# Optimization experiments

Hardware: AMD Instinct MI355X
Metric: run time of the kernel (lower is better)

Reference implementation:

```python
import jax, jax.numpy as jnp
import numpy as np

T, B, F, H = 1024, 128, 243, 20  # timesteps, batch, feature dim, hidden dim
POOL = 4  # MaxPool1d(4, 4) over the 512 channel axis -> 128


def setup_inputs() -> dict:
    key = jax.random.key(0)
    ks = jax.random.split(key, 9)
    s = lambda fan_in: 1.0 / np.sqrt(fan_in)
    return {
        "feats": jax.random.normal(ks[0], (T, B * POOL, F), dtype=jnp.float32),
        "e0": jax.random.normal(ks[1], (B, H), dtype=jnp.float32),
        # PyTorch GRUCell params: gates stacked as [r; z; n]
        "W_ih": jax.random.uniform(ks[2], (3 * H, F), jnp.float32, -s(H), s(H)),
        "W_hh": jax.random.uniform(ks[3], (3 * H, H), jnp.float32, -s(H), s(H)),
        "b_ih": jax.random.uniform(ks[4], (3 * H,), jnp.float32, -s(H), s(H)),
        "b_hh": jax.random.uniform(ks[5], (3 * H,), jnp.float32, -s(H), s(H)),
        # decoder: Linear(20, 243) + ReLU
        "W_dec": jax.random.uniform(ks[6], (F, H), jnp.float32, -s(H), s(H)),
        "b_dec": jax.random.uniform(ks[7], (F,), jnp.float32, -s(H), s(H)),
    }


def reference(feats, e0, W_ih, W_hh, b_ih, b_hh, W_dec, b_dec):
    # temporal max-pool over the 512 axis (kernel=4, stride=4) -> [T, B, F]
    h_seq = feats.reshape(T, B, POOL, F).max(axis=2)
    # precompute input-gate projections once (vectorized over T): [T, B, 3H]
    x_gates = jnp.einsum('tbf,gf->tbg', h_seq, W_ih) + b_ih

    def step(e, inp):
        h_t, xg = inp
        hg = e @ W_hh.T + b_hh
        xr, xz, xn = jnp.split(xg, 3, axis=-1)
        hr, hz, hn = jnp.split(hg, 3, axis=-1)
        r = jax.nn.sigmoid(xr + hr)
        z = jax.nn.sigmoid(xz + hz)
        n = jnp.tanh(xn + r * hn)
        e_new = (1.0 - z) * n + z * e
        fo = jax.nn.relu(e_new @ W_dec.T + b_dec)
        loss = jnp.mean((fo - h_t) ** 2)
        return e_new, loss

    _, losses = jax.lax.scan(step, e0, (h_seq, x_gates))
    return jnp.mean(losses)  # sum(loss_list) / step
```

## Files before the change

kernel.cpp:

```cpp
#include <hip/hip_runtime.h>
#include <cstddef>

#define T_ 1024
#define B_ 128
#define F_ 243
#define H_ 20
#define G_ 60
#define R_ 512
#define P_ 8
#define FP_ 256
#define HS_ 244

__device__ __forceinline__ float rdlane(float v, int l) {
  return __int_as_float(__builtin_amdgcn_readlane(__float_as_int(v), l));
}
#define RCP(x) __builtin_amdgcn_rcpf(x)
#if __has_builtin(__builtin_amdgcn_exp2f)
#define EXP2(x) __builtin_amdgcn_exp2f(x)
#else
#define EXP2(x) __expf((x) * 0.6931471805599453f)
#endif
#define NL2E_ -1.4426950408889634f
#define L2E2_ 2.8853900817779268f

__global__ __launch_bounds__(256) void k1a_pool(
    const float* __restrict__ feats, float* __restrict__ h_seq,
    const float* __restrict__ W_ih, float* __restrict__ Wt)
{
  const int bid = blockIdx.x;
  if (bid < 60) {
    const int i = bid * 256 + threadIdx.x;
    if (i < FP_ * G_) {
      const int f = i / G_, g = i - f * G_;
      Wt[(size_t)f * G_ + g] = (f < F_) ? W_ih[(size_t)g * F_ + f] : 0.f;
    }
  }
  const int t = bid & (T_ - 1);
  const int b0 = (bid >> 10) << 3;
  const int col = threadIdx.x;
  if (col < F_) {
    #pragma unroll
    for (int bb = 0; bb < 8; ++bb) {
      const float* p =
          feats + ((size_t)t * R_ + (size_t)(b0 + bb) * 4) * F_ + col;
      const float v =
          fmaxf(fmaxf(p[0], p[F_]), fmaxf(p[2 * F_], p[3 * F_]));
      h_seq[((size_t)(b0 + bb) * T_ + t) * HS_ + col] = v;
    }
  }
}

__global__ __launch_bounds__(256) void k1b_gemm(
    const float* __restrict__ h_seq, const float* __restrict__ Wt,
    const float* __restrict__ b_ih, float* __restrict__ xg)
{
  __shared__ __align__(16) float Ws[64 * 60];
  const int bid = blockIdx.x;
  const int b = bid >> 4;
  const int t0 = (bid & 15) << 6;
  const int tid = threadIdx.x;
  const int rg = tid >> 4;
  const int gcol = tid & 15;
  const int gc4 = (gcol < 15) ? gcol * 4 : 56;
  const float* hsb = h_seq + ((size_t)b * T_ + t0) * HS_;

  float acc[4][4];
  #pragma unroll
  for (int i = 0; i < 4; ++i)
    #pragma unroll
    for (int j = 0; j < 4; ++j) acc[i][j] = 0.f;

  for (int c = 0; c < 4; ++c) {
    const int FC = c * 64;
    __syncthreads();
    for (int j = tid; j < 64 * 60; j += 256)
      Ws[j] = Wt[(size_t)FC * G_ + j];
    __syncthreads();
    #pragma unroll
    for (int fj = 0; fj < 16; ++fj) {
      const float* wp = &Ws[(fj * 4) * 60 + gc4];
      const float4 w0 = *(const float4*)(wp);
      const float4 w1 = *(const float4*)(wp + 60);
      const float4 w2 = *(const float4*)(wp + 120);
      const float4 w3 = *(const float4*)(wp + 180);
      #pragma unroll
      for (int i = 0; i < 4; ++i) {
        const int row = (rg << 2) + i;
        const float4 a4 =
            *(const float4*)&hsb[(size_t)row * HS_ + FC + fj * 4];
        acc[i][0] = fmaf(a4.x, w0.x, fmaf(a4.y, w1.x, fmaf(a4.z, w2.x, fmaf(a4.w, w3.x, acc[i][0]))));
        acc[i][1] = fmaf(a4.x, w0.y, fmaf(a4.y, w1.y, fmaf(a4.z, w2.y, fmaf(a4.w, w3.y, acc[i][1]))));
        acc[i][2] = fmaf(a4.x, w0.z, fmaf(a4.y, w1.z, fmaf(a4.z, w2.z, fmaf(a4.w, w3.z, acc[i][2]))));
        acc[i][3] = fmaf(a4.x, w0.w, fmaf(a4.y, w1.w, fmaf(a4.z, w2.w, fmaf(a4.w, w3.w, acc[i][3]))));
      }
    }
  }

  if (gcol < 15) {
    const float4 bi4 = *(const float4*)&b_ih[gc4];
    #pragma unroll
    for (int i = 0; i < 4; ++i) {
      const int row = (rg << 2) + i;
      float4 o;
      o.x = acc[i][0] + bi4.x;  o.y = acc[i][1] + bi4.y;
      o.z = acc[i][2] + bi4.z;  o.w = acc[i][3] + bi4.w;
      *(float4*)&xg[((size_t)b * T_ + t0 + row) * G_ + gc4] = o;
    }
  }
}

__global__ __launch_bounds__(64) void k2_recur(
    const float* __restrict__ e0, const float* __restrict__ W_hh,
    const float* __restrict__ b_hh, const float* xg,
    float* e_store, float* __restrict__ ehead)
{
  const int b = blockIdx.x;
  const int lane = threadIdx.x;
  const bool own = lane < H_;
  const int j0 = own ? lane : 0;

  float2 wr2[10], wz2[10], wn2[10];
  #pragma unroll
  for (int k = 0; k < 10; ++k) {
    wr2[k] = *(const float2*)&W_hh[j0 * H_ + 2 * k];
    wz2[k] = *(const float2*)&W_hh[(j0 + 20) * H_ + 2 * k];
    wn2[k] = *(const float2*)&W_hh[(j0 + 40) * H_ + 2 * k];
  }
  const float bhr = b_hh[j0], bhz = b_hh[j0 + 20], bhn = b_hh[j0 + 40];

  float e_own = e0[b * H_ + j0];
  float2 es2[10];
  #pragma unroll
  for (int k = 0; k < 10; ++k) {
    es2[k].x = rdlane(e_own, 2 * k);
    es2[k].y = rdlane(e_own, 2 * k + 1);
  }

  const float* xgb = xg + (size_t)b * T_ * G_;
  float* xslab = e_store + (size_t)b * T_ * G_;
  float* ehb = ehead + b * (P_ * H_);

  float xr[P_], xz[P_], xn[P_];
  #pragma unroll
  for (int j = 0; j < P_; ++j) {
    xr[j] = xgb[(size_t)j * G_ + j0];
    xz[j] = xgb[(size_t)j * G_ + j0 + 20];
    xn[j] = xgb[(size_t)j * G_ + j0 + 40];
  }

#define STEP(j, RELOAD)                                                    \
  {                                                                        \
    const int t = t0 + (j);                                                \
    const float xrv = xr[j], xzv = xz[j], xnv = xn[j];                     \
    if (RELOAD) {                                                          \
      const float* xp = xgb + (size_t)(t + P_) * G_;                       \
      xr[j] = xp[j0]; xz[j] = xp[j0 + 20]; xn[j] = xp[j0 + 40];            \
    }                                                                      \
    float2 rA = make_float2(bhr, 0.f), rB = make_float2(0.f, 0.f);         \
    float2 zA = make_float2(bhz, 0.f), zB = make_float2(0.f, 0.f);         \
    float2 nA = make_float2(bhn, 0.f), nB = make_float2(0.f, 0.f);         \
    _Pragma("unroll")                                                      \
    for (int k = 0; k < 5; ++k) {                                          \
      rA = wr2[k] * es2[k] + rA;   rB = wr2[k + 5] * es2[k + 5] + rB;      \
      zA = wz2[k] * es2[k] + zA;   zB = wz2[k + 5] * es2[k + 5] + zB;      \
      nA = wn2[k] * es2[k] + nA;   nB = wn2[k + 5] * es2[k + 5] + nB;      \
    }                                                                      \
    const float hr = (rA.x + rB.x) + (rA.y + rB.y);                        \
    const float hz = (zA.x + zB.x) + (zA.y + zB.y);                        \
    const float hn = (nA.x + nB.x) + (nA.y + nB.y);                        \
    const float rg = RCP(1.f + EXP2((xrv + hr) * NL2E_));                  \
    const float zg = RCP(1.f + EXP2((xzv + hz) * NL2E_));                  \
    const float aa = fmaf(rg, hn, xnv);                                    \
    const float ng = 1.f - 2.f * RCP(EXP2(aa * L2E2_) + 1.f);              \
    const float enew = fmaf(zg, e_own - ng, ng);                           \
    if (own) {                                                             \
      float* dst = (t >= P_) ? (xslab + (size_t)(t - P_) * H_ + lane)      \
                             : (ehb + t * H_ + lane);                      \
      *dst = enew;                                                         \
    }                                                                      \
    e_own = enew;                                                          \
    _Pragma("unroll")                                                      \
    for (int k = 0; k < 10; ++k) {                                         \
      es2[k].x = rdlane(enew, 2 * k);                                      \
      es2[k].y = rdlane(enew, 2 * k + 1);                                  \
    }                                                                      \
  }

  for (int t0 = 0; t0 < T_ - P_; t0 += P_) {
    STEP(0, true) STEP(1, true) STEP(2, true) STEP(3, true)
    STEP(4, true) STEP(5, true) STEP(6, true) STEP(7, true)
  }
  {
    const int t0 = T_ - P_;
    STEP(0, false) STEP(1, false) STEP(2, false) STEP(3, false)
    STEP(4, false) STEP(5, false) STEP(6, false) STEP(7, false)
  }
#undef STEP
}

#define K4_ROWS 128
__global__ __launch_bounds__(256) void k4_decode(
    const float* __restrict__ W_dec, const float* __restrict__ b_dec,
    const float* __restrict__ h_seq, const float* __restrict__ e_store,
    const float* __restrict__ ehead, float* __restrict__ partials)
{
  __shared__ float elds[K4_ROWS * H_];
  __shared__ float red[4];
  const int tid = threadIdx.x;
  const int f = tid;
  const bool act = f < F_;
  const int lane = tid & 63, wave = tid >> 6;
  const size_t r0 = (size_t)blockIdx.x * K4_ROWS;
  const int b = (int)(r0 >> 10);
  const int t0 = (int)(r0 & (T_ - 1));
  const float* xslab = e_store + (size_t)b * T_ * G_;
  const float* ehb = ehead + b * (P_ * H_);

  for (int i = tid; i < K4_ROWS * H_; i += 256) {
    const int trow = i / H_;
    const int c = i - trow * H_;
    const int t = t0 + trow;
    elds[i] = (t >= P_) ? xslab[(size_t)(t - P_) * H_ + c] : ehb[t * H_ + c];
  }

  float wd[H_];
  float bd = 0.f;
  if (act) {
    #pragma unroll
    for (int k = 0; k < H_; ++k) wd[k] = W_dec[f * H_ + k];
    bd = b_dec[f];
  }
  __syncthreads();

  float acc = 0.f;
  #pragma unroll 2
  for (int i = 0; i < K4_ROWS; ++i) {
    const float2* ep = (const float2*)&elds[i * H_];
    float d = bd;
    #pragma unroll
    for (int k = 0; k < 10; ++k) {
      const float2 e2 = ep[k];
      d = fmaf(wd[2 * k], e2.x, fmaf(wd[2 * k + 1], e2.y, d));
    }
    const float fo = fmaxf(d, 0.f);
    if (act) {
      const float h = h_seq[(r0 + i) * HS_ + f];
      const float df = fo - h;
      acc = fmaf(df, df, acc);
    }
  }

  #pragma unroll
  for (int m = 32; m >= 1; m >>= 1) acc += __shfl_xor(acc, m);
  if (lane == 0) red[wave] = acc;
  __syncthreads();
  if (tid == 0) partials[blockIdx.x] = red[0] + red[1] + red[2] + red[3];
}

__global__ __launch_bounds__(64) void k3_reduce(
    const float* __restrict__ partials, float* __restrict__ out)
{
  const int lane = threadIdx.x;
  float a = 0.f;
  #pragma unroll
  for (int i = 0; i < 16; ++i) a += partials[i * 64 + lane];
  #pragma unroll
  for (int m = 32; m >= 1; m >>= 1) a += __shfl_xor(a, m);
  if (lane == 0) out[0] = a * (float)(1.0 / ((double)T_ * B_ * F_));
}

extern "C" void kernel_launch(void* const* d_in, const int* in_sizes, int n_in,
                              void* d_out, int out_size, void* d_ws, size_t ws_size,
                              hipStream_t stream) {
  const float* feats = (const float*)d_in[0];
  const float* e0    = (const float*)d_in[1];
  const float* W_ih  = (const float*)d_in[2];
  const float* W_hh  = (const float*)d_in[3];
  const float* b_ih  = (const float*)d_in[4];
  const float* b_hh  = (const float*)d_in[5];
  const float* W_dec = (const float*)d_in[6];
  const float* b_dec = (const float*)d_in[7];
  float* out = (float*)d_out;

  float* ws = (float*)d_ws;
  float* h_seq    = ws;
  float* xgates   = ws + (size_t)B_ * T_ * HS_;
  float* partials = xgates + (size_t)T_ * B_ * G_;
  float* ehead    = partials + 1024;
  float* Wt       = ehead + B_ * P_ * H_;

  hipLaunchKernelGGL(k1a_pool, dim3(T_ * (B_ / 8)), dim3(256), 0, stream,
                     feats, h_seq, W_ih, Wt);
  hipLaunchKernelGGL(k1b_gemm, dim3(B_ * 16), dim3(256), 0, stream,
                     h_seq, Wt, b_ih, xgates);
  hipLaunchKernelGGL(k2_recur, dim3(B_), dim3(64), 0, stream,
                     e0, W_hh, b_hh, xgates, xgates, ehead);
  hipLaunchKernelGGL(k4_decode, dim3((T_ * B_) / K4_ROWS), dim3(256), 0, stream,
                     W_dec, b_dec, h_seq, xgates, ehead, partials);
  hipLaunchKernelGGL(k3_reduce, dim3(1), dim3(64), 0, stream,
                     partials, out);
}
```

Measured before the change: 495.9 us.

## Fuse decoder loss into recurrence kernel using producer/consumer waves and LDS double buffer

The separate decode kernel is merged into the recurrence kernel. Wave 0 runs the GRU recurrence and writes each 8-step chunk of hidden states into a double-buffered LDS tile, while four consumer waves compute the decoder output and squared error for that chunk. This removes the global store and reload of the hidden-state sequence and one kernel launch. The cost is a block-wide barrier every 8 steps on the serial critical path, and the decode work is now spread over only 128 blocks.

```diff
diff --git a/kernel.cpp b/kernel.cpp
--- a/kernel.cpp
+++ b/kernel.cpp
@@ -109,144 +109,133 @@
   }
 }
 
-__global__ __launch_bounds__(64) void k2_recur(
+__global__ __launch_bounds__(320) void k2_fused(
     const float* __restrict__ e0, const float* __restrict__ W_hh,
-    const float* __restrict__ b_hh, const float* xg,
-    float* e_store, float* __restrict__ ehead)
-{
+    const float* __restrict__ b_hh, const float* __restrict__ xg,
+    const float* __restrict__ h_seq, const float* __restrict__ W_dec,
+    const float* __restrict__ b_dec, float* __restrict__ partials)
+{
+  __shared__ float ebuf[2][P_][H_];
+  __shared__ float red[8];
   const int b = blockIdx.x;
-  const int lane = threadIdx.x;
-  const bool own = lane < H_;
-  const int j0 = own ? lane : 0;
-
-  float2 wr2[10], wz2[10], wn2[10];
-  #pragma unroll
-  for (int k = 0; k < 10; ++k) {
-    wr2[k] = *(const float2*)&W_hh[j0 * H_ + 2 * k];
-    wz2[k] = *(const float2*)&W_hh[(j0 + 20) * H_ + 2 * k];
-    wn2[k] = *(const float2*)&W_hh[(j0 + 40) * H_ + 2 * k];
-  }
-  const float bhr = b_hh[j0], bhz = b_hh[j0 + 20], bhn = b_hh[j0 + 40];
-
-  float e_own = e0[b * H_ + j0];
-  float2 es2[10];
-  #pragma unroll
-  for (int k = 0; k < 10; ++k) {
-    es2[k].x = rdlane(e_own, 2 * k);
-    es2[k].y = rdlane(e_own, 2 * k + 1);
-  }
-
-  const float* xgb = xg + (size_t)b * T_ * G_;
-  float* xslab = e_store + (size_t)b * T_ * G_;
-  float* ehb = ehead + b * (P_ * H_);
-
-  float xr[P_], xz[P_], xn[P_];
-  #pragma unroll
-  for (int j = 0; j < P_; ++j) {
-    xr[j] = xgb[(size_t)j * G_ + j0];
-    xz[j] = xgb[(size_t)j * G_ + j0 + 20];
-    xn[j] = xgb[(size_t)j * G_ + j0 + 40];
-  }
+  const int tid = threadIdx.x;
+  const int lane = tid & 63;
+  const int wave = tid >> 6;
+  float acc = 0.f;
+
+  if (wave == 0) {
+    const bool own = lane < H_;
+    const int j0 = own ? lane : 0;
+
+    float2 wr2[10], wz2[10], wn2[10];
+    #pragma unroll
+    for (int k = 0; k < 10; ++k) {
+      wr2[k] = *(const float2*)&W_hh[j0 * H_ + 2 * k];
+      wz2[k] = *(const float2*)&W_hh[(j0 + 20) * H_ + 2 * k];
+      wn2[k] = *(const float2*)&W_hh[(j0 + 40) * H_ + 2 * k];
+    }
+    const float bhr = b_hh[j0], bhz = b_hh[j0 + 20], bhn = b_hh[j0 + 40];
+
+    float e_own = e0[b * H_ + j0];
+    float2 es2[10];
+    #pragma unroll
+    for (int k = 0; k < 10; ++k) {
+      es2[k].x = rdlane(e_own, 2 * k);
+      es2[k].y = rdlane(e_own, 2 * k + 1);
+    }
+
+    const float* xgb = xg + (size_t)b * T_ * G_;
+    float xr[P_], xz[P_], xn[P_];
+    #pragma unroll
+    for (int j = 0; j < P_; ++j) {
+      xr[j] = xgb[(size_t)j * G_ + j0];
+      xz[j] = xgb[(size_t)j * G_ + j0 + 20];
+      xn[j] = xgb[(size_t)j * G_ + j0 + 40];
+    }
 
 #define STEP(j, RELOAD)                                                    \
-  {                                                                        \
-    const int t = t0 + (j);                                                \
-    const float xrv = xr[j], xzv = xz[j], xnv = xn[j];                     \
-    if (RELOAD) {                                                          \
-      const float* xp = xgb + (size_t)(t + P_) * G_;                       \
-      xr[j] = xp[j0]; xz[j] = xp[j0 + 20]; xn[j] = xp[j0 + 40];            \
-    }                                                                      \
-    float2 rA = make_float2(bhr, 0.f), rB = make_float2(0.f, 0.f);         \
-    float2 zA = make_float2(bhz, 0.f), zB = make_float2(0.f, 0.f);         \
-    float2 nA = make_float2(bhn, 0.f), nB = make_float2(0.f, 0.f);         \
-    _Pragma("unroll")                                                      \
-    for (int k = 0; k < 5; ++k) {                                          \
-      rA = wr2[k] * es2[k] + rA;   rB = wr2[k + 5] * es2[k + 5] + rB;      \
-      zA = wz2[k] * es2[k] + zA;   zB = wz2[k + 5] * es2[k + 5] + zB;      \
-      nA = wn2[k] * es2[k] + nA;   nB = wn2[k + 5] * es2[k + 5] + nB;      \
-    }                                                                      \
-    const float hr = (rA.x + rB.x) + (rA.y + rB.y);                        \
-    const float hz = (zA.x + zB.x) + (zA.y + zB.y);                        \
-    const float hn = (nA.x + nB.x) + (nA.y + nB.y);                        \
-    const float rg = RCP(1.f + EXP2((xrv + hr) * NL2E_));                  \
-    const float zg = RCP(1.f + EXP2((xzv + hz) * NL2E_));                  \
-    const float aa = fmaf(rg, hn, xnv);                                    \
-    const float ng = 1.f - 2.f * RCP(EXP2(aa * L2E2_) + 1.f);              \
-    const float enew = fmaf(zg, e_own - ng, ng);                           \
-    if (own) {                                                             \
-      float* dst = (t >= P_) ? (xslab + (size_t)(t - P_) * H_ + lane)      \
-                             : (ehb + t * H_ + lane);                      \
-      *dst = enew;                                                         \
-    }                                                                      \
-    e_own = enew;                                                          \
-    _Pragma("unroll")                                                      \
-    for (int k = 0; k < 10; ++k) {                                         \
-      es2[k].x = rdlane(enew, 2 * k);                                      \
-      es2[k].y = rdlane(enew, 2 * k + 1);                                  \
-    }                                                                      \
-  }
-
-  for (int t0 = 0; t0 < T_ - P_; t0 += P_) {
-    STEP(0, true) STEP(1, true) STEP(2, true) STEP(3, true)
-    STEP(4, true) STEP(5, true) STEP(6, true) STEP(7, true)
-  }
-  {
-    const int t0 = T_ - P_;
-    STEP(0, false) STEP(1, false) STEP(2, false) STEP(3, false)
-    STEP(4, false) STEP(5, false) STEP(6, false) STEP(7, false)
-  }
+    {                                                                      \
+      const int t = t0 + (j);                                              \
+      const float xrv = xr[j], xzv = xz[j], xnv = xn[j];                   \
+      if (RELOAD) {                                                        \
+        const float* xp = xgb + (size_t)(t + P_) * G_;                     \
+        xr[j] = xp[j0]; xz[j] = xp[j0 + 20]; xn[j] = xp[j0 + 40];          \
+      }                                                                    \
+      float2 rA = make_float2(bhr, 0.f), rB = make_float2(0.f, 0.f);       \
+      float2 zA = make_float2(bhz, 0.f), zB = make_float2(0.f, 0.f);       \
+      float2 nA = make_float2(bhn, 0.f), nB = make_float2(0.f, 0.f);       \
+      _Pragma("unroll")                                                    \
+      for (int k = 0; k < 5; ++k) {                                        \
+        rA = wr2[k] * es2[k] + rA;   rB = wr2[k + 5] * es2[k + 5] + rB;    \
+        zA = wz2[k] * es2[k] + zA;   zB = wz2[k + 5] * es2[k + 5] + zB;    \
+        nA = wn2[k] * es2[k] + nA;   nB = wn2[k + 5] * es2[k + 5] + nB;    \
+      }                                                                    \
+      const float hr = (rA.x + rB.x) + (rA.y + rB.y);                      \
+      const float hz = (zA.x + zB.x) + (zA.y + zB.y);                      \
+      const float hn = (nA.x + nB.x) + (nA.y + nB.y);                      \
+      const float rg = RCP(1.f + EXP2((xrv + hr) * NL2E_));                \
+      const float zg = RCP(1.f + EXP2((xzv + hz) * NL2E_));                \
+      const float aa = fmaf(rg, hn, xnv);                                  \
+      const float ng = 1.f - 2.f * RCP(EXP2(aa * L2E2_) + 1.f);            \
+      const float enew = fmaf(zg, e_own - ng, ng);                         \
+      if (own) ebuf[(t0 >> 3) & 1][j][lane] = enew;                        \
+      e_own = enew;                                                        \
+      _Pragma("unroll")                                                    \
+      for (int k = 0; k < 10; ++k) {                                       \
+        es2[k].x = rdlane(enew, 2 * k);                                    \
+        es2[k].y = rdlane(enew, 2 * k + 1);                                \
+      }                                                                    \
+    }
+
+    for (int t0 = 0; t0 < T_ - P_; t0 += P_) {
+      STEP(0, true) STEP(1, true) STEP(2, true) STEP(3, true)
+      STEP(4, true) STEP(5, true) STEP(6, true) STEP(7, true)
+      __syncthreads();
+    }
+    {
+      const int t0 = T_ - P_;
+      STEP(0, false) STEP(1, false) STEP(2, false) STEP(3, false)
+      STEP(4, false) STEP(5, false) STEP(6, false) STEP(7, false)
+      __syncthreads();
+    }
 #undef STEP
-}
-
-#define K4_ROWS 128
-__global__ __launch_bounds__(256) void k4_decode(
-    const float* __restrict__ W_dec, const float* __restrict__ b_dec,
-    const float* __restrict__ h_seq, const float* __restrict__ e_store,
-    const float* __restrict__ ehead, float* __restrict__ partials)
-{
-  __shared__ float elds[K4_ROWS * H_];
-  __shared__ float red[4];
-  const int tid = threadIdx.x;
-  const int f = tid;
-  const bool act = f < F_;
-  const int lane = tid & 63, wave = tid >> 6;
-  const size_t r0 = (size_t)blockIdx.x * K4_ROWS;
-  const int b = (int)(r0 >> 10);
-  const int t0 = (int)(r0 & (T_ - 1));
-  const float* xslab = e_store + (size_t)b * T_ * G_;
-  const float* ehb = ehead + b * (P_ * H_);
-
-  for (int i = tid; i < K4_ROWS * H_; i += 256) {
-    const int trow = i / H_;
-    const int c = i - trow * H_;
-    const int t = t0 + trow;
-    elds[i] = (t >= P_) ? xslab[(size_t)(t - P_) * H_ + c] : ehb[t * H_ + c];
-  }
-
-  float wd[H_];
-  float bd = 0.f;
-  if (act) {
+  } else {
+    const int ct = tid - 64;
+    const bool act = ct < F_;
+    const int f = act ? ct : 0;
+    float wd[H_];
     #pragma unroll
     for (int k = 0; k < H_; ++k) wd[k] = W_dec[f * H_ + k];
-    bd = b_dec[f];
-  }
-  __syncthreads();
-
-  float acc = 0.f;
-  #pragma unroll 2
-  for (int i = 0; i < K4_ROWS; ++i) {
-    const float2* ep = (const float2*)&elds[i * H_];
-    float d = bd;
-    #pragma unroll
-    for (int k = 0; k < 10; ++k) {
-      const float2 e2 = ep[k];
-      d = fmaf(wd[2 * k], e2.x, fmaf(wd[2 * k + 1], e2.y, d));
-    }
-    const float fo = fmaxf(d, 0.f);
-    if (act) {
-      const float h = h_seq[(r0 + i) * HS_ + f];
-      const float df = fo - h;
-      acc = fmaf(df, df, acc);
+    const float bd = b_dec[f];
+    const float* hsb = h_seq + (size_t)b * T_ * HS_;
+
+    float hcur[P_], hnxt[P_];
+    #pragma unroll
+    for (int j = 0; j < P_; ++j) hcur[j] = hsb[(size_t)j * HS_ + f];
+
+    for (int g = 0; g < T_ / P_; ++g) {
+      __syncthreads();
+      if (g < T_ / P_ - 1) {
+        #pragma unroll
+        for (int j = 0; j < P_; ++j)
+          hnxt[j] = hsb[(size_t)(P_ * (g + 1) + j) * HS_ + f];
+      }
+      const float* eb = &ebuf[g & 1][0][0];
+      #pragma unroll
+      for (int j = 0; j < P_; ++j) {
+        const float2* ep = (const float2*)&eb[j * H_];
+        float d = bd;
+        #pragma unroll
+        for (int k = 0; k < 10; ++k) {
+          const float2 e2 = ep[k];
+          d = fmaf(wd[2 * k], e2.x, fmaf(wd[2 * k + 1], e2.y, d));
+        }
+        const float fo = fmaxf(d, 0.f);
+        const float df = fo - hcur[j];
+        if (act) acc = fmaf(df, df, acc);
+      }
+      #pragma unroll
+      for (int j = 0; j < P_; ++j) hcur[j] = hnxt[j];
     }
   }
 
@@ -254,16 +243,15 @@
   for (int m = 32; m >= 1; m >>= 1) acc += __shfl_xor(acc, m);
   if (lane == 0) red[wave] = acc;
   __syncthreads();
-  if (tid == 0) partials[blockIdx.x] = red[0] + red[1] + red[2] + red[3];
+  if (tid == 0)
+    partials[b] = ((red[0] + red[1]) + (red[2] + red[3])) + red[4];
 }
 
 __global__ __launch_bounds__(64) void k3_reduce(
     const float* __restrict__ partials, float* __restrict__ out)
 {
   const int lane = threadIdx.x;
-  float a = 0.f;
-  #pragma unroll
-  for (int i = 0; i < 16; ++i) a += partials[i * 64 + lane];
+  float a = partials[lane] + partials[lane + 64];
   #pragma unroll
   for (int m = 32; m >= 1; m >>= 1) a += __shfl_xor(a, m);
   if (lane == 0) out[0] = a * (float)(1.0 / ((double)T_ * B_ * F_));
@@ -285,18 +273,15 @@
   float* ws = (float*)d_ws;
   float* h_seq    = ws;
   float* xgates   = ws + (size_t)B_ * T_ * HS_;
-  float* partials = xgates + (size_t)T_ * B_ * G_;
-  float* ehead    = partials + 1024;
-  float* Wt       = ehead + B_ * P_ * H_;
+  float* partials = xgates + (size_t)B_ * T_ * G_;
+  float* Wt       = partials + 128;
 
   hipLaunchKernelGGL(k1a_pool, dim3(T_ * (B_ / 8)), dim3(256), 0, stream,
                      feats, h_seq, W_ih, Wt);
   hipLaunchKernelGGL(k1b_gemm, dim3(B_ * 16), dim3(256), 0, stream,
                      h_seq, Wt, b_ih, xgates);
-  hipLaunchKernelGGL(k2_recur, dim3(B_), dim3(64), 0, stream,
-                     e0, W_hh, b_hh, xgates, xgates, ehead);
-  hipLaunchKernelGGL(k4_decode, dim3((T_ * B_) / K4_ROWS), dim3(256), 0, stream,
-                     W_dec, b_dec, h_seq, xgates, ehead, partials);
+  hipLaunchKernelGGL(k2_fused, dim3(B_), dim3(320), 0, stream,
+                     e0, W_hh, b_hh, xgates, h_seq, W_dec, b_dec, partials);
   hipLaunchKernelGGL(k3_reduce, dim3(1), dim3(64), 0, stream,
                      partials, out);
 }
```

Result: faster. 452.8 us (-8.7%).
